# Performance work log

Hardware: AMD Instinct MI355X
Metric: run time of the kernel (lower is better)

Reference implementation:

```python
import jax, jax.numpy as jnp
import numpy as np

NUM_EXPS = [8, 16, 64, 256, 1024]
KS = [4, 4, 32, 32, 256]
HIDDEN = 256
OUT_DIM = 3
IN_DIM = 2
N_IMGS = 2
N_COORDS = 1024


def setup_inputs() -> dict:
    key = jax.random.key(0)
    ks = jax.random.split(key, 16)
    inp = {}
    inp["raw_gates"] = jax.random.normal(ks[0], (N_IMGS, sum(NUM_EXPS)), jnp.float32)
    inp["coords"] = jax.random.uniform(ks[1], (N_COORDS, IN_DIM), jnp.float32, -1.0, 1.0)
    fan_in = [IN_DIM] + [HIDDEN] * 4
    fan_out = [HIDDEN * e for e in NUM_EXPS[:-1]] + [OUT_DIM * NUM_EXPS[-1]]
    for i, (fi, fo) in enumerate(zip(fan_in, fan_out)):
        # first_layer_sine_init / sine_init weight scales from the torch module
        bound = (1.0 / fi) if i == 0 else (np.sqrt(6.0 / fi) / 30.0)
        inp[f"W{i}"] = jax.random.uniform(ks[2 + 2 * i], (fo, fi), jnp.float32, -bound, bound)
        bb = 1.0 / np.sqrt(fi)  # torch nn.Linear default bias init
        inp[f"b{i}"] = jax.random.uniform(ks[3 + 2 * i], (fo,), jnp.float32, -bb, bb)
    return inp


def _topk_gate(g, k):
    # torch: topk(|g|, k+1) -> keep top k, gather signed values, scatter into zeros
    _, idx = jax.lax.top_k(jnp.abs(g), min(k + 1, g.shape[1]))
    idx = idx[:, :k]
    vals = jnp.take_along_axis(g, idx, axis=1)
    rows = jnp.arange(g.shape[0])[:, None]
    return jnp.zeros_like(g).at[rows, idx].set(vals)


def _forward(raw_gates, coords, Ws, bs):
    offs = np.cumsum([0] + NUM_EXPS)
    gates = [_topk_gate(raw_gates[:, offs[i]:offs[i + 1]], KS[i]) for i in range(len(NUM_EXPS))]
    Ni = raw_gates.shape[0]
    Nc = coords.shape[0]
    E0 = NUM_EXPS[0]
    # layer 0: shared experts, combine = sparse gates @ expert outputs (== MoECombiner scatter-add)
    h = jnp.sin(30.0 * (coords @ Ws[0].T + bs[0]))            # [Nc, H*E0]
    h = h.reshape(Nc, HIDDEN, E0).transpose(2, 0, 1).reshape(E0, Nc * HIDDEN)  # [E0, Nc*H]
    x = (gates[0] @ h).reshape(Ni, Nc, HIDDEN)                # [Ni, Nc, H]
    for i in range(1, len(NUM_EXPS)):
        E = NUM_EXPS[i]
        h = x @ Ws[i].T + bs[i]                               # [Ni, Nc, d*E]
        if i < len(NUM_EXPS) - 1:
            h = jnp.sin(30.0 * h)
            d = HIDDEN
        else:
            d = OUT_DIM                                       # last layer: no activation
        h = h.reshape(Ni, Nc, d, E)
        x = jnp.einsum('icde,ie->icd', h, gates[i])           # bmm(gate, experts)
    return x


def reference(raw_gates, coords, W0, b0, W1, b1, W2, b2, W3, b3, W4, b4):
    return _forward(raw_gates, coords, (W0, W1, W2, W3, W4), (b0, b1, b2, b3, b4))
```

## Files before the change

kernel.cpp:

```cpp
#include <hip/hip_runtime.h>
#include <math.h>

#define NC 1024
#define HID 256
#define NI 2

typedef _Float16 f16x8 __attribute__((ext_vector_type(8)));
typedef float f32x4 __attribute__((ext_vector_type(4)));
using gvoid = __attribute__((address_space(1))) const void;
using lvoid = __attribute__((address_space(3))) void;

#define LO_SCALE 2048.0f
#define LO_INV (1.0f / 2048.0f)

__global__ __launch_bounds__(1024) void gate_kernel(const float* __restrict__ rg,
                                                    int* __restrict__ gidx,
                                                    float* __restrict__ gval)
{
    const int EDAT[5] = {8, 16, 64, 256, 1024};
    const int KDAT[5] = {4, 4, 32, 32, 256};
    const int OFF[5]  = {0, 8, 24, 88, 344};
    const int level = blockIdx.x, img = blockIdx.y;
    const int E = EDAT[level], K = KDAT[level], off = OFF[level];
    __shared__ float ga[1024];
    const float* src = rg + img * 1368 + off;
    const int t = threadIdx.x;
    if (t < E) ga[t] = src[t];
    __syncthreads();
    if (t < E) {
        const float v = ga[t];
        const float a = fabsf(v);
        int rank = 0;
#pragma unroll 8
        for (int j = 0; j < E; j++) {
            float aj = fabsf(ga[j]);
            rank += (aj > a) || (aj == a && j < t);
        }
        if (rank < K) {
            int base = (level * 2 + img) * 256;
            gidx[base + rank] = t;
            gval[base + rank] = v;
        }
    }
}

__global__ __launch_bounds__(256) void layer0_kernel(const float* __restrict__ coords,
                                                     const float* __restrict__ W0,
                                                     const float* __restrict__ b0,
                                                     const int* __restrict__ gidx,
                                                     const float* __restrict__ gval,
                                                     float* __restrict__ xout)
{
    const int c = blockIdx.x, img = blockIdx.y, h = threadIdx.x;
    __shared__ int gi[4];
    __shared__ float gv[4];
    if (h < 4) {
        int base = (0 * 2 + img) * 256;
        gi[h] = gidx[base + h];
        gv[h] = gval[base + h];
    }
    __syncthreads();
    const float c0 = coords[c * 2], c1 = coords[c * 2 + 1];
    float s = 0.f;
#pragma unroll
    for (int k = 0; k < 4; k++) {
        int row = h * 8 + gi[k];
        s += gv[k] * __sinf(30.f * (c0 * W0[row * 2] + c1 * W0[row * 2 + 1] + b0[row]));
    }
    xout[((size_t)img * NC + c) * HID + h] = s;
}

__global__ __launch_bounds__(256) void xpack_kernel(const float* __restrict__ x,
                                                    _Float16* __restrict__ Ap)
{
    const int mt = blockIdx.x, img = blockIdx.y, sa = blockIdx.z;
    const int t = threadIdx.x;
    const int c = t & 63, r0 = t >> 6;
    const float* xb = x + ((size_t)img * NC + mt * 64) * HID;
    _Float16* aph = Ap + ((size_t)(img * 16 + mt) * 8 + sa) * 4096;
    _Float16* apl = aph + 4 * 4096;
    const int kk = sa * 64 + c;
#pragma unroll
    for (int rr = 0; rr < 64; rr += 4) {
        int r = rr + r0;
        float v = xb[r * HID + kk];
        _Float16 h = (_Float16)v;
        int idx = r * 64 + (c ^ ((r & 7) << 3));
        aph[idx] = h;
        apl[idx] = (_Float16)((v - (float)h) * LO_SCALE);
    }
}

__global__ __launch_bounds__(256) void wpack_kernel(const float* __restrict__ W,
                                                    const float* __restrict__ bias,
                                                    const int* __restrict__ gidx,
                                                    const float* __restrict__ gval,
                                                    int level, int E, int lgK,
                                                    _Float16* __restrict__ Bp,
                                                    float* __restrict__ biasP,
                                                    float* __restrict__ gvP,
                                                    int ntiles)
{
    const int ntile = blockIdx.x, img = blockIdx.y, sa = blockIdx.z;
    const int t = threadIdx.x;
    const int N = ntiles * 64;
    __shared__ int wrowS[64];
    const int base = (level * 2 + img) * 256;
    if (t < 64) {
        int n = ntile * 64 + t;
        int dd = n >> lgK, k = n & ((1 << lgK) - 1);
        int wrow = dd * E + gidx[base + k];
        wrowS[t] = wrow;
        if (sa == 0) {
            biasP[img * N + n] = bias[wrow];
            gvP[img * N + n] = gval[base + k];
        }
    }
    __syncthreads();
    const int c = t & 63, r0 = t >> 6;
    const int kk = sa * 64 + c;
    _Float16* bph = Bp + ((size_t)(img * ntiles + ntile) * 8 + sa) * 4096;
    _Float16* bpl = bph + 4 * 4096;
#pragma unroll
    for (int rr = 0; rr < 64; rr += 4) {
        int r = rr + r0;
        float v = W[(size_t)wrowS[r] * HID + kk];
        _Float16 h = (_Float16)v;
        int idx = r * 64 + (c ^ ((r & 7) << 3));
        bph[idx] = h;
        bpl[idx] = (_Float16)((v - (float)h) * LO_SCALE);
    }
}

template <int KGRP, int NTB>
__global__ __launch_bounds__(256, 1) void mid_mfma_kernel(const _Float16* __restrict__ Ap,
                                                          const _Float16* __restrict__ Bp,
                                                          const float* __restrict__ biasP,
                                                          const float* __restrict__ gvP,
                                                          float* __restrict__ x_out)
{
    constexpr int NTBX = NTB / 8;
    const int b = blockIdx.x;
    const int q = b & 7;
    const int j = b >> 3;
    const int mtp = j & 7;
    const int img = (j >> 3) & 1;
    const int ntl = j >> 4;
    const int nt = q * NTBX + ntl;

    const int tid = threadIdx.x;
    const int wave = tid >> 6, lane = tid & 63;
    const int wm = wave & 1, wn = wave >> 1;
    const int l15 = lane & 15, lhi = lane >> 4;

    __shared__ __align__(16) char lds[131072];
    float* S = (float*)lds;

    const int ntiles = NTB * 2;
    const int N = NTB * 128;
    const _Float16* ag = Ap + ((size_t)(img * 16 + mtp * 2) * 8) * 4096;
    const _Float16* bg = Bp + ((size_t)(img * ntiles + nt * 2) * 8) * 4096;

    const _Float16* sbase = (wave & 2) ? bg : ag;
    const int planeAdd = (wave & 1) ? 4 : 0;
    auto stage = [&](int bufoff, int p) {
#pragma unroll
        for (int qq = 0; qq < 16; ++qq) {
            const _Float16* g = sbase + (size_t)(qq >> 3) * 32768
                              + (planeAdd + p) * 4096 + (qq & 7) * 512 + lane * 8;
            __builtin_amdgcn_global_load_lds((gvoid*)g,
                (lvoid*)(lds + bufoff + wave * 16384 + qq * 1024), 16, 0, 0);
        }
    };

    f32x4 acc[4][4], accL[4][4];
#pragma unroll
    for (int mi = 0; mi < 4; mi++)
#pragma unroll
        for (int ni = 0; ni < 4; ni++) { acc[mi][ni] = (f32x4)0.f; accL[mi][ni] = (f32x4)0.f; }

    stage(0, 0);

#pragma unroll
    for (int p = 0; p < 4; ++p) {
        const int cur = (p & 1) * 65536;
        asm volatile("s_waitcnt vmcnt(0)" ::: "memory");
        __syncthreads();
        if (p < 3) stage(65536 - cur, p + 1);

#pragma unroll
        for (int ks = 0; ks < 2; ++ks) {
            f16x8 ah[4], al[4], bh[4], bl[4];
#pragma unroll
            for (int mi = 0; mi < 4; ++mi) {
                int row = wm * 64 + mi * 16 + l15;
                int off = (row >> 6) * 8192 + (row & 63) * 128
                        + (((lhi + 4 * ks) ^ (row & 7)) * 16);
                ah[mi] = *(const f16x8*)(lds + cur + off);
                al[mi] = *(const f16x8*)(lds + cur + 16384 + off);
            }
#pragma unroll
            for (int ni = 0; ni < 4; ++ni) {
                int row = wn * 64 + ni * 16 + l15;
                int off = (row >> 6) * 8192 + (row & 63) * 128
                        + (((lhi + 4 * ks) ^ (row & 7)) * 16);
                bh[ni] = *(const f16x8*)(lds + cur + 32768 + off);
                bl[ni] = *(const f16x8*)(lds + cur + 49152 + off);
            }
#pragma unroll
            for (int mi = 0; mi < 4; ++mi)
#pragma unroll
                for (int ni = 0; ni < 4; ++ni)
                    acc[mi][ni] = __builtin_amdgcn_mfma_f32_16x16x32_f16(ah[mi], bh[ni],
                                                                         acc[mi][ni], 0, 0, 0);
#pragma unroll
            for (int mi = 0; mi < 4; ++mi)
#pragma unroll
                for (int ni = 0; ni < 4; ++ni)
                    accL[mi][ni] = __builtin_amdgcn_mfma_f32_16x16x32_f16(al[mi], bh[ni],
                                                                          accL[mi][ni], 0, 0, 0);
#pragma unroll
            for (int mi = 0; mi < 4; ++mi)
#pragma unroll
                for (int ni = 0; ni < 4; ++ni)
                    accL[mi][ni] = __builtin_amdgcn_mfma_f32_16x16x32_f16(ah[mi], bl[ni],
                                                                          accL[mi][ni], 0, 0, 0);
        }
    }
    __syncthreads();

#pragma unroll
    for (int mi = 0; mi < 4; ++mi)
#pragma unroll
        for (int ni = 0; ni < 4; ++ni) {
            int n = wn * 64 + ni * 16 + l15;
            int gn = nt * 128 + n;
            float bv = biasP[img * N + gn];
            float gv = gvP[img * N + gn];
#pragma unroll
            for (int r = 0; r < 4; ++r) {
                int m = wm * 64 + mi * 16 + lhi * 4 + r;
                float val = acc[mi][ni][r] + accL[mi][ni][r] * LO_INV;
                S[m * 129 + n] = gv * __sinf(30.f * (val + bv));
            }
        }
    __syncthreads();

    float* xo = x_out + ((size_t)img * NC + mtp * 128) * HID;
    if (KGRP == 32) {
#pragma unroll
        for (int rep = 0; rep < 2; ++rep) {
            int idx = rep * 256 + tid;
            int m = idx >> 2, d = idx & 3;
            float s = 0.f;
#pragma unroll
            for (int jj = 0; jj < 32; ++jj) s += S[m * 129 + d * 32 + ((jj + d * 8) & 31)];
            xo[m * HID + nt * 4 + d] = s;
        }
    } else {
#pragma unroll
        for (int rep = 0; rep < 16; ++rep) {
            int idx = rep * 256 + tid;
            int m = idx >> 5, dl = idx & 31;
            const float* Sp = S + m * 129 + dl * 4;
            xo[m * HID + nt * 32 + dl] = Sp[0] + Sp[1] + Sp[2] + Sp[3];
        }
    }
}

__global__ __launch_bounds__(256) void l4combine_kernel(const float* __restrict__ W4,
                                                        const float* __restrict__ b4,
                                                        const int* __restrict__ gidx,
                                                        const float* __restrict__ gval,
                                                        float* __restrict__ Weff,
                                                        float* __restrict__ beff)
{
    const int d = blockIdx.x, img = blockIdx.y;
    const int t = threadIdx.x;
    const int base = (4 * 2 + img) * 256;
    __shared__ int rows[256];
    __shared__ float gs[256];
    __shared__ float bred[256];
    int e = gidx[base + t];
    float g = gval[base + t];
    rows[t] = (d * 1024 + e) * 256;
    gs[t] = g;
    bred[t] = g * b4[d * 1024 + e];
    __syncthreads();
    float acc = 0.f;
#pragma unroll 4
    for (int k = 0; k < 256; ++k)
        acc = fmaf(gs[k], W4[(size_t)rows[k] + t], acc);
    Weff[(img * 3 + d) * 256 + t] = acc;
    for (int s = 128; s > 0; s >>= 1) {
        if (t < s) bred[t] += bred[t + s];
        __syncthreads();
    }
    if (t == 0) beff[img * 3 + d] = bred[0];
}

__global__ __launch_bounds__(256) void l4apply_kernel(const float* __restrict__ x_in,
                                                      const float* __restrict__ Weff,
                                                      const float* __restrict__ beff,
                                                      float* __restrict__ out)
{
    const int img = blockIdx.y;
    const int c = blockIdx.x * 256 + threadIdx.x;
    __shared__ float ws[3][256];
    __shared__ float bs[3];
    const int t = threadIdx.x;
    if (t < 192) {
        int d = t / 64, k4 = t % 64;
        *(float4*)&ws[d][k4 * 4] = *(const float4*)(Weff + (img * 3 + d) * 256 + k4 * 4);
    }
    if (t < 3) bs[t] = beff[img * 3 + t];
    __syncthreads();
    const float* xb = x_in + ((size_t)img * NC + c) * HID;
    float a0 = 0.f, a1 = 0.f, a2 = 0.f;
#pragma unroll 4
    for (int k = 0; k < 256; k += 4) {
        const float4 xv = *(const float4*)(xb + k);
        const float4 w0 = *(const float4*)&ws[0][k];
        const float4 w1 = *(const float4*)&ws[1][k];
        const float4 w2 = *(const float4*)&ws[2][k];
        a0 += xv.x * w0.x + xv.y * w0.y + xv.z * w0.z + xv.w * w0.w;
        a1 += xv.x * w1.x + xv.y * w1.y + xv.z * w1.z + xv.w * w1.w;
        a2 += xv.x * w2.x + xv.y * w2.y + xv.z * w2.z + xv.w * w2.w;
    }
    float* o = out + ((size_t)img * NC + c) * 3;
    o[0] = a0 + bs[0];
    o[1] = a1 + bs[1];
    o[2] = a2 + bs[2];
}

extern "C" void kernel_launch(void* const* d_in, const int* in_sizes, int n_in,
                              void* d_out, int out_size, void* d_ws, size_t ws_size,
                              hipStream_t stream)
{
    const float* rg     = (const float*)d_in[0];
    const float* coords = (const float*)d_in[1];
    const float* W0 = (const float*)d_in[2];
    const float* b0 = (const float*)d_in[3];
    const float* W1 = (const float*)d_in[4];
    const float* b1 = (const float*)d_in[5];
    const float* W2 = (const float*)d_in[6];
    const float* b2 = (const float*)d_in[7];
    const float* W3 = (const float*)d_in[8];
    const float* b3 = (const float*)d_in[9];
    const float* W4 = (const float*)d_in[10];
    const float* b4 = (const float*)d_in[11];
    float* out = (float*)d_out;

    char* ws = (char*)d_ws;
    int*      gidx  = (int*)ws;
    float*    gval  = (float*)(ws + 10240);
    float*    xA    = (float*)(ws + 20480);
    float*    xB    = (float*)(ws + 2117632);
    _Float16* Ap    = (_Float16*)(ws + 4214784);
    _Float16* Bp    = (_Float16*)(ws + 6311936);
    float*    biasP = (float*)(ws + 23089152);
    float*    gvP   = (float*)(ws + 23154688);
    float*    Weff  = (float*)(ws + 23220224);
    float*    beff  = (float*)(ws + 23228416);

    gate_kernel<<<dim3(5, 2), 1024, 0, stream>>>(rg, gidx, gval);
    l4combine_kernel<<<dim3(3, 2), 256, 0, stream>>>(W4, b4, gidx, gval, Weff, beff);
    layer0_kernel<<<dim3(NC, NI), 256, 0, stream>>>(coords, W0, b0, gidx, gval, xA);

    xpack_kernel<<<dim3(16, 2, 4), 256, 0, stream>>>(xA, Ap);
    wpack_kernel<<<dim3(16, 2, 4), 256, 0, stream>>>(W1, b1, gidx, gval, 1, 16, 2, Bp, biasP, gvP, 16);
    mid_mfma_kernel<4, 8><<<128, 256, 0, stream>>>(Ap, Bp, biasP, gvP, xB);

    xpack_kernel<<<dim3(16, 2, 4), 256, 0, stream>>>(xB, Ap);
    wpack_kernel<<<dim3(128, 2, 4), 256, 0, stream>>>(W2, b2, gidx, gval, 2, 64, 5, Bp, biasP, gvP, 128);
    mid_mfma_kernel<32, 64><<<1024, 256, 0, stream>>>(Ap, Bp, biasP, gvP, xA);

    xpack_kernel<<<dim3(16, 2, 4), 256, 0, stream>>>(xA, Ap);
    wpack_kernel<<<dim3(128, 2, 4), 256, 0, stream>>>(W3, b3, gidx, gval, 3, 256, 5, Bp, biasP, gvP, 128);
    mid_mfma_kernel<32, 64><<<1024, 256, 0, stream>>>(Ap, Bp, biasP, gvP, xB);

    l4apply_kernel<<<dim3(4, 2), 256, 0, stream>>>(xB, Weff, beff, out);
}
```

Before: 312.7 us.

## Fuse activation packing into epilogues, batch weight packing, and single-buffer MFMA LDS

Layer0 and the MFMA epilogues now write the hi/lo fp16 swizzled A-operand directly, which removes the separate xpack kernels and their fp32 round trips. Weight packing for W1/W2 and the layer-4 weight combine are merged into one prep kernel, with the combine split across chunks and accumulated through atomics into buffers that the gate kernel zeroes. The MFMA kernel drops from 128KB of double-buffered LDS to a 64KB single buffer and stages the next panel after the second k-step's fragments are read. The epilogue reduction moves from an LDS scratch pass to warp shuffles. These changes cut kernel launches and memory traffic, but the single buffer gives less load/compute overlap, and the float atomics make the summation order nondeterministic.

```diff
diff --git a/kernel.cpp b/kernel.cpp
--- a/kernel.cpp
+++ b/kernel.cpp
@@ -13,9 +13,38 @@
 #define LO_SCALE 2048.0f
 #define LO_INV (1.0f / 2048.0f)
 
+#define OFF_GIDX  0
+#define OFF_GVAL  10240
+#define OFF_B1    20480
+#define OFF_G1    28672
+#define OFF_B2    36864
+#define OFF_G2    102400
+#define OFF_B3    167936
+#define OFF_G3    233472
+#define OFF_WEFF  299008
+#define OFF_BEFF  305152
+#define OFF_APA   307200
+#define OFF_APB   (OFF_APA + 2097152)
+#define OFF_BP1   (OFF_APB + 2097152)
+#define OFF_BP23  (OFF_BP1 + 2097152)
+
+__device__ __forceinline__ void pack_store(_Float16* __restrict__ ApN, int img,
+                                           int m, int h, float v)
+{
+    _Float16 hi = (_Float16)v;
+    _Float16 lo = (_Float16)((v - (float)hi) * LO_SCALE);
+    int mt = m >> 6, r = m & 63;
+    size_t base = ((size_t)(img * 16 + mt) * 8 + (h >> 6)) * 4096
+                + r * 64 + ((h & 63) ^ ((r & 7) << 3));
+    ApN[base] = hi;
+    ApN[base + 16384] = lo;
+}
+
 __global__ __launch_bounds__(1024) void gate_kernel(const float* __restrict__ rg,
                                                     int* __restrict__ gidx,
-                                                    float* __restrict__ gval)
+                                                    float* __restrict__ gval,
+                                                    float* __restrict__ Weff,
+                                                    float* __restrict__ beff)
 {
     const int EDAT[5] = {8, 16, 64, 256, 1024};
     const int KDAT[5] = {4, 4, 32, 32, 256};
@@ -25,6 +54,10 @@
     __shared__ float ga[1024];
     const float* src = rg + img * 1368 + off;
     const int t = threadIdx.x;
+    if (level == 0) {
+        if (t < 768) Weff[img * 768 + t] = 0.f;
+        if (t < 3) beff[img * 3 + t] = 0.f;
+    }
     if (t < E) ga[t] = src[t];
     __syncthreads();
     if (t < E) {
@@ -49,7 +82,7 @@
                                                      const float* __restrict__ b0,
                                                      const int* __restrict__ gidx,
                                                      const float* __restrict__ gval,
-                                                     float* __restrict__ xout)
+                                                     _Float16* __restrict__ ApN)
 {
     const int c = blockIdx.x, img = blockIdx.y, h = threadIdx.x;
     __shared__ int gi[4];
@@ -67,41 +100,19 @@
         int row = h * 8 + gi[k];
         s += gv[k] * __sinf(30.f * (c0 * W0[row * 2] + c1 * W0[row * 2 + 1] + b0[row]));
     }
-    xout[((size_t)img * NC + c) * HID + h] = s;
-}
-
-__global__ __launch_bounds__(256) void xpack_kernel(const float* __restrict__ x,
-                                                    _Float16* __restrict__ Ap)
-{
-    const int mt = blockIdx.x, img = blockIdx.y, sa = blockIdx.z;
-    const int t = threadIdx.x;
-    const int c = t & 63, r0 = t >> 6;
-    const float* xb = x + ((size_t)img * NC + mt * 64) * HID;
-    _Float16* aph = Ap + ((size_t)(img * 16 + mt) * 8 + sa) * 4096;
-    _Float16* apl = aph + 4 * 4096;
-    const int kk = sa * 64 + c;
-#pragma unroll
-    for (int rr = 0; rr < 64; rr += 4) {
-        int r = rr + r0;
-        float v = xb[r * HID + kk];
-        _Float16 h = (_Float16)v;
-        int idx = r * 64 + (c ^ ((r & 7) << 3));
-        aph[idx] = h;
-        apl[idx] = (_Float16)((v - (float)h) * LO_SCALE);
-    }
-}
-
-__global__ __launch_bounds__(256) void wpack_kernel(const float* __restrict__ W,
-                                                    const float* __restrict__ bias,
-                                                    const int* __restrict__ gidx,
-                                                    const float* __restrict__ gval,
-                                                    int level, int E, int lgK,
-                                                    _Float16* __restrict__ Bp,
-                                                    float* __restrict__ biasP,
-                                                    float* __restrict__ gvP,
-                                                    int ntiles)
-{
-    const int ntile = blockIdx.x, img = blockIdx.y, sa = blockIdx.z;
+    pack_store(ApN, img, c, h, s);
+}
+
+__device__ __forceinline__ void wpack_body(const float* __restrict__ W,
+                                           const float* __restrict__ bias,
+                                           const int* __restrict__ gidx,
+                                           const float* __restrict__ gval,
+                                           int level, int E, int lgK, int ntiles,
+                                           _Float16* __restrict__ Bp,
+                                           float* __restrict__ biasP,
+                                           float* __restrict__ gvP,
+                                           int ntile, int img, int sa)
+{
     const int t = threadIdx.x;
     const int N = ntiles * 64;
     __shared__ int wrowS[64];
@@ -132,12 +143,76 @@
     }
 }
 
-template <int KGRP, int NTB>
+__global__ __launch_bounds__(256) void prep_kernel(const float* __restrict__ W1,
+                                                   const float* __restrict__ b1,
+                                                   const float* __restrict__ W2,
+                                                   const float* __restrict__ b2,
+                                                   const float* __restrict__ W4,
+                                                   const float* __restrict__ b4,
+                                                   const int* __restrict__ gidx,
+                                                   const float* __restrict__ gval,
+                                                   _Float16* __restrict__ Bp1,
+                                                   float* __restrict__ bias1,
+                                                   float* __restrict__ gv1,
+                                                   _Float16* __restrict__ Bp23,
+                                                   float* __restrict__ bias2,
+                                                   float* __restrict__ gv2,
+                                                   float* __restrict__ Weff,
+                                                   float* __restrict__ beff)
+{
+    const int b = blockIdx.x;
+    if (b < 128) {
+        int ntile = b & 15, img = (b >> 4) & 1, sa = b >> 5;
+        wpack_body(W1, b1, gidx, gval, 1, 16, 2, 16, Bp1, bias1, gv1, ntile, img, sa);
+    } else if (b < 1152) {
+        int s = b - 128;
+        int ntile = s & 127, img = (s >> 7) & 1, sa = s >> 8;
+        wpack_body(W2, b2, gidx, gval, 2, 64, 5, 128, Bp23, bias2, gv2, ntile, img, sa);
+    } else {
+        const int idx = b - 1152;
+        const int d = idx % 3, img = (idx / 3) % 2, ck = idx / 6;
+        const int t = threadIdx.x;
+        __shared__ float gs[32];
+        __shared__ int rows[32];
+        const int base = (4 * 2 + img) * 256 + ck * 32;
+        if (t < 32) {
+            gs[t] = gval[base + t];
+            rows[t] = (d * 1024 + gidx[base + t]) * 256;
+        }
+        __syncthreads();
+        float acc = 0.f;
+#pragma unroll 8
+        for (int k = 0; k < 32; ++k)
+            acc = fmaf(gs[k], W4[(size_t)rows[k] + t], acc);
+        atomicAdd(&Weff[(img * 3 + d) * 256 + t], acc);
+        if (t == 0) {
+            float bb = 0.f;
+            for (int k = 0; k < 32; ++k)
+                bb += gs[k] * b4[d * 1024 + gidx[base + k]];
+            atomicAdd(&beff[img * 3 + d], bb);
+        }
+    }
+}
+
+__global__ __launch_bounds__(256) void wpack3_kernel(const float* __restrict__ W,
+                                                     const float* __restrict__ bias,
+                                                     const int* __restrict__ gidx,
+                                                     const float* __restrict__ gval,
+                                                     _Float16* __restrict__ Bp,
+                                                     float* __restrict__ biasP,
+                                                     float* __restrict__ gvP)
+{
+    wpack_body(W, bias, gidx, gval, 3, 256, 5, 128, Bp, biasP, gvP,
+               blockIdx.x, blockIdx.y, blockIdx.z);
+}
+
+template <int KGRP, int NTB, bool PACK>
 __global__ __launch_bounds__(256, 1) void mid_mfma_kernel(const _Float16* __restrict__ Ap,
                                                           const _Float16* __restrict__ Bp,
-                                                          const float* __restrict__ biasP,
-                                                          const float* __restrict__ gvP,
-                                                          float* __restrict__ x_out)
+                                                          const float* __restrict__ biasPp,
+                                                          const float* __restrict__ gvPp,
+                                                          float* __restrict__ xout,
+                                                          _Float16* __restrict__ ApN)
 {
     constexpr int NTBX = NTB / 8;
     const int b = blockIdx.x;
@@ -153,8 +228,7 @@
     const int wm = wave & 1, wn = wave >> 1;
     const int l15 = lane & 15, lhi = lane >> 4;
 
-    __shared__ __align__(16) char lds[131072];
-    float* S = (float*)lds;
+    __shared__ __align__(16) char lds[65536];
 
     const int ntiles = NTB * 2;
     const int N = NTB * 128;
@@ -163,13 +237,13 @@
 
     const _Float16* sbase = (wave & 2) ? bg : ag;
     const int planeAdd = (wave & 1) ? 4 : 0;
-    auto stage = [&](int bufoff, int p) {
+    auto stage = [&](int p) {
 #pragma unroll
         for (int qq = 0; qq < 16; ++qq) {
             const _Float16* g = sbase + (size_t)(qq >> 3) * 32768
                               + (planeAdd + p) * 4096 + (qq & 7) * 512 + lane * 8;
             __builtin_amdgcn_global_load_lds((gvoid*)g,
-                (lvoid*)(lds + bufoff + wave * 16384 + qq * 1024), 16, 0, 0);
+                (lvoid*)(lds + wave * 16384 + qq * 1024), 16, 0, 0);
         }
     };
 
@@ -179,124 +253,163 @@
 #pragma unroll
         for (int ni = 0; ni < 4; ni++) { acc[mi][ni] = (f32x4)0.f; accL[mi][ni] = (f32x4)0.f; }
 
-    stage(0, 0);
+    stage(0);
 
 #pragma unroll
     for (int p = 0; p < 4; ++p) {
-        const int cur = (p & 1) * 65536;
         asm volatile("s_waitcnt vmcnt(0)" ::: "memory");
         __syncthreads();
-        if (p < 3) stage(65536 - cur, p + 1);
-
-#pragma unroll
-        for (int ks = 0; ks < 2; ++ks) {
-            f16x8 ah[4], al[4], bh[4], bl[4];
-#pragma unroll
-            for (int mi = 0; mi < 4; ++mi) {
-                int row = wm * 64 + mi * 16 + l15;
-                int off = (row >> 6) * 8192 + (row & 63) * 128
-                        + (((lhi + 4 * ks) ^ (row & 7)) * 16);
-                ah[mi] = *(const f16x8*)(lds + cur + off);
-                al[mi] = *(const f16x8*)(lds + cur + 16384 + off);
-            }
-#pragma unroll
-            for (int ni = 0; ni < 4; ++ni) {
-                int row = wn * 64 + ni * 16 + l15;
-                int off = (row >> 6) * 8192 + (row & 63) * 128
-                        + (((lhi + 4 * ks) ^ (row & 7)) * 16);
-                bh[ni] = *(const f16x8*)(lds + cur + 32768 + off);
-                bl[ni] = *(const f16x8*)(lds + cur + 49152 + off);
-            }
+        f16x8 ah[2][4], al[2][4], bh[2][4], bl[2][4];
+#pragma unroll
+        for (int mi = 0; mi < 4; ++mi) {
+            int row = wm * 64 + mi * 16 + l15;
+            int off = (row >> 6) * 8192 + (row & 63) * 128 + ((lhi ^ (row & 7)) * 16);
+            ah[0][mi] = *(const f16x8*)(lds + off);
+            al[0][mi] = *(const f16x8*)(lds + 16384 + off);
+        }
+#pragma unroll
+        for (int ni = 0; ni < 4; ++ni) {
+            int row = wn * 64 + ni * 16 + l15;
+            int off = (row >> 6) * 8192 + (row & 63) * 128 + ((lhi ^ (row & 7)) * 16);
+            bh[0][ni] = *(const f16x8*)(lds + 32768 + off);
+            bl[0][ni] = *(const f16x8*)(lds + 49152 + off);
+        }
+#pragma unroll
+        for (int mi = 0; mi < 4; ++mi)
+#pragma unroll
+            for (int ni = 0; ni < 4; ++ni)
+                acc[mi][ni] = __builtin_amdgcn_mfma_f32_16x16x32_f16(ah[0][mi], bh[0][ni],
+                                                                     acc[mi][ni], 0, 0, 0);
+#pragma unroll
+        for (int mi = 0; mi < 4; ++mi)
+#pragma unroll
+            for (int ni = 0; ni < 4; ++ni)
+                accL[mi][ni] = __builtin_amdgcn_mfma_f32_16x16x32_f16(al[0][mi], bh[0][ni],
+                                                                      accL[mi][ni], 0, 0, 0);
+#pragma unroll
+        for (int mi = 0; mi < 4; ++mi)
+#pragma unroll
+            for (int ni = 0; ni < 4; ++ni)
+                accL[mi][ni] = __builtin_amdgcn_mfma_f32_16x16x32_f16(ah[0][mi], bl[0][ni],
+                                                                      accL[mi][ni], 0, 0, 0);
+#pragma unroll
+        for (int mi = 0; mi < 4; ++mi) {
+            int row = wm * 64 + mi * 16 + l15;
+            int off = (row >> 6) * 8192 + (row & 63) * 128 + ((((lhi + 4)) ^ (row & 7)) * 16);
+            ah[1][mi] = *(const f16x8*)(lds + off);
+            al[1][mi] = *(const f16x8*)(lds + 16384 + off);
+        }
+#pragma unroll
+        for (int ni = 0; ni < 4; ++ni) {
+            int row = wn * 64 + ni * 16 + l15;
+            int off = (row >> 6) * 8192 + (row & 63) * 128 + ((((lhi + 4)) ^ (row & 7)) * 16);
+            bh[1][ni] = *(const f16x8*)(lds + 32768 + off);
+            bl[1][ni] = *(const f16x8*)(lds + 49152 + off);
+        }
+        __syncthreads();
+        if (p < 3) stage(p + 1);
+#pragma unroll
+        for (int mi = 0; mi < 4; ++mi)
+#pragma unroll
+            for (int ni = 0; ni < 4; ++ni)
+                acc[mi][ni] = __builtin_amdgcn_mfma_f32_16x16x32_f16(ah[1][mi], bh[1][ni],
+                                                                     acc[mi][ni], 0, 0, 0);
+#pragma unroll
+        for (int mi = 0; mi < 4; ++mi)
+#pragma unroll
+            for (int ni = 0; ni < 4; ++ni)
+                accL[mi][ni] = __builtin_amdgcn_mfma_f32_16x16x32_f16(al[1][mi], bh[1][ni],
+                                                                      accL[mi][ni], 0, 0, 0);
+#pragma unroll
+        for (int mi = 0; mi < 4; ++mi)
+#pragma unroll
+            for (int ni = 0; ni < 4; ++ni)
+                accL[mi][ni] = __builtin_amdgcn_mfma_f32_16x16x32_f16(ah[1][mi], bl[1][ni],
+                                                                      accL[mi][ni], 0, 0, 0);
+    }
+
+    const int mbase = mtp * 128 + wm * 64;
+    if (KGRP == 32) {
+        float red[4][2][4];
+#pragma unroll
+        for (int mi = 0; mi < 4; ++mi)
+#pragma unroll
+            for (int pp = 0; pp < 2; ++pp)
+#pragma unroll
+                for (int r = 0; r < 4; ++r) red[mi][pp][r] = 0.f;
+#pragma unroll
+        for (int ni = 0; ni < 4; ++ni) {
+            int gn = nt * 128 + wn * 64 + ni * 16 + l15;
+            float bv = biasPp[img * N + gn];
+            float gvv = gvPp[img * N + gn];
+#pragma unroll
+            for (int mi = 0; mi < 4; ++mi)
+#pragma unroll
+                for (int r = 0; r < 4; ++r) {
+                    float val = acc[mi][ni][r] + accL[mi][ni][r] * LO_INV;
+                    red[mi][ni >> 1][r] += gvv * __sinf(30.f * (val + bv));
+                }
+        }
+#pragma unroll
+        for (int mask = 1; mask <= 8; mask <<= 1)
+#pragma unroll
+            for (int mi = 0; mi < 4; ++mi)
+#pragma unroll
+                for (int pp = 0; pp < 2; ++pp)
+#pragma unroll
+                    for (int r = 0; r < 4; ++r)
+                        red[mi][pp][r] += __shfl_xor(red[mi][pp][r], mask);
+        if (l15 == 0) {
+#pragma unroll
+            for (int mi = 0; mi < 4; ++mi)
+#pragma unroll
+                for (int pp = 0; pp < 2; ++pp)
+#pragma unroll
+                    for (int r = 0; r < 4; ++r) {
+                        int m = mbase + mi * 16 + lhi * 4 + r;
+                        int h = nt * 4 + wn * 2 + pp;
+                        if (PACK) pack_store(ApN, img, m, h, red[mi][pp][r]);
+                        else xout[((size_t)img * NC + m) * HID + h] = red[mi][pp][r];
+                    }
+        }
+    } else {
+        float e[4][4][4];
+#pragma unroll
+        for (int ni = 0; ni < 4; ++ni) {
+            int gn = nt * 128 + wn * 64 + ni * 16 + l15;
+            float bv = biasPp[img * N + gn];
+            float gvv = gvPp[img * N + gn];
+#pragma unroll
+            for (int mi = 0; mi < 4; ++mi)
+#pragma unroll
+                for (int r = 0; r < 4; ++r) {
+                    float val = acc[mi][ni][r] + accL[mi][ni][r] * LO_INV;
+                    e[mi][ni][r] = gvv * __sinf(30.f * (val + bv));
+                }
+        }
+#pragma unroll
+        for (int mask = 1; mask <= 2; mask <<= 1)
 #pragma unroll
             for (int mi = 0; mi < 4; ++mi)
 #pragma unroll
                 for (int ni = 0; ni < 4; ++ni)
-                    acc[mi][ni] = __builtin_amdgcn_mfma_f32_16x16x32_f16(ah[mi], bh[ni],
-                                                                         acc[mi][ni], 0, 0, 0);
+#pragma unroll
+                    for (int r = 0; r < 4; ++r)
+                        e[mi][ni][r] += __shfl_xor(e[mi][ni][r], mask);
+        if ((l15 & 3) == 0) {
 #pragma unroll
             for (int mi = 0; mi < 4; ++mi)
 #pragma unroll
                 for (int ni = 0; ni < 4; ++ni)
-                    accL[mi][ni] = __builtin_amdgcn_mfma_f32_16x16x32_f16(al[mi], bh[ni],
-                                                                          accL[mi][ni], 0, 0, 0);
-#pragma unroll
-            for (int mi = 0; mi < 4; ++mi)
-#pragma unroll
-                for (int ni = 0; ni < 4; ++ni)
-                    accL[mi][ni] = __builtin_amdgcn_mfma_f32_16x16x32_f16(ah[mi], bl[ni],
-                                                                          accL[mi][ni], 0, 0, 0);
-        }
-    }
-    __syncthreads();
-
-#pragma unroll
-    for (int mi = 0; mi < 4; ++mi)
-#pragma unroll
-        for (int ni = 0; ni < 4; ++ni) {
-            int n = wn * 64 + ni * 16 + l15;
-            int gn = nt * 128 + n;
-            float bv = biasP[img * N + gn];
-            float gv = gvP[img * N + gn];
-#pragma unroll
-            for (int r = 0; r < 4; ++r) {
-                int m = wm * 64 + mi * 16 + lhi * 4 + r;
-                float val = acc[mi][ni][r] + accL[mi][ni][r] * LO_INV;
-                S[m * 129 + n] = gv * __sinf(30.f * (val + bv));
-            }
-        }
-    __syncthreads();
-
-    float* xo = x_out + ((size_t)img * NC + mtp * 128) * HID;
-    if (KGRP == 32) {
-#pragma unroll
-        for (int rep = 0; rep < 2; ++rep) {
-            int idx = rep * 256 + tid;
-            int m = idx >> 2, d = idx & 3;
-            float s = 0.f;
-#pragma unroll
-            for (int jj = 0; jj < 32; ++jj) s += S[m * 129 + d * 32 + ((jj + d * 8) & 31)];
-            xo[m * HID + nt * 4 + d] = s;
-        }
-    } else {
-#pragma unroll
-        for (int rep = 0; rep < 16; ++rep) {
-            int idx = rep * 256 + tid;
-            int m = idx >> 5, dl = idx & 31;
-            const float* Sp = S + m * 129 + dl * 4;
-            xo[m * HID + nt * 32 + dl] = Sp[0] + Sp[1] + Sp[2] + Sp[3];
-        }
-    }
-}
-
-__global__ __launch_bounds__(256) void l4combine_kernel(const float* __restrict__ W4,
-                                                        const float* __restrict__ b4,
-                                                        const int* __restrict__ gidx,
-                                                        const float* __restrict__ gval,
-                                                        float* __restrict__ Weff,
-                                                        float* __restrict__ beff)
-{
-    const int d = blockIdx.x, img = blockIdx.y;
-    const int t = threadIdx.x;
-    const int base = (4 * 2 + img) * 256;
-    __shared__ int rows[256];
-    __shared__ float gs[256];
-    __shared__ float bred[256];
-    int e = gidx[base + t];
-    float g = gval[base + t];
-    rows[t] = (d * 1024 + e) * 256;
-    gs[t] = g;
-    bred[t] = g * b4[d * 1024 + e];
-    __syncthreads();
-    float acc = 0.f;
-#pragma unroll 4
-    for (int k = 0; k < 256; ++k)
-        acc = fmaf(gs[k], W4[(size_t)rows[k] + t], acc);
-    Weff[(img * 3 + d) * 256 + t] = acc;
-    for (int s = 128; s > 0; s >>= 1) {
-        if (t < s) bred[t] += bred[t + s];
-        __syncthreads();
-    }
-    if (t == 0) beff[img * 3 + d] = bred[0];
+#pragma unroll
+                    for (int r = 0; r < 4; ++r) {
+                        int m = mbase + mi * 16 + lhi * 4 + r;
+                        int h = nt * 32 + wn * 16 + ni * 4 + (l15 >> 2);
+                        if (PACK) pack_store(ApN, img, m, h, e[mi][ni][r]);
+                        else xout[((size_t)img * NC + m) * HID + h] = e[mi][ni][r];
+                    }
+        }
+    }
 }
 
 __global__ __launch_bounds__(256) void l4apply_kernel(const float* __restrict__ x_in,
@@ -352,32 +465,31 @@
     float* out = (float*)d_out;
 
     char* ws = (char*)d_ws;
-    int*      gidx  = (int*)ws;
-    float*    gval  = (float*)(ws + 10240);
-    float*    xA    = (float*)(ws + 20480);
-    float*    xB    = (float*)(ws + 2117632);
-    _Float16* Ap    = (_Float16*)(ws + 4214784);
-    _Float16* Bp    = (_Float16*)(ws + 6311936);
-    float*    biasP = (float*)(ws + 23089152);
-    float*    gvP   = (float*)(ws + 23154688);
-    float*    Weff  = (float*)(ws + 23220224);
-    float*    beff  = (float*)(ws + 23228416);
-
-    gate_kernel<<<dim3(5, 2), 1024, 0, stream>>>(rg, gidx, gval);
-    l4combine_kernel<<<dim3(3, 2), 256, 0, stream>>>(W4, b4, gidx, gval, Weff, beff);
-    layer0_kernel<<<dim3(NC, NI), 256, 0, stream>>>(coords, W0, b0, gidx, gval, xA);
-
-    xpack_kernel<<<dim3(16, 2, 4), 256, 0, stream>>>(xA, Ap);
-    wpack_kernel<<<dim3(16, 2, 4), 256, 0, stream>>>(W1, b1, gidx, gval, 1, 16, 2, Bp, biasP, gvP, 16);
-    mid_mfma_kernel<4, 8><<<128, 256, 0, stream>>>(Ap, Bp, biasP, gvP, xB);
-
-    xpack_kernel<<<dim3(16, 2, 4), 256, 0, stream>>>(xB, Ap);
-    wpack_kernel<<<dim3(128, 2, 4), 256, 0, stream>>>(W2, b2, gidx, gval, 2, 64, 5, Bp, biasP, gvP, 128);
-    mid_mfma_kernel<32, 64><<<1024, 256, 0, stream>>>(Ap, Bp, biasP, gvP, xA);
-
-    xpack_kernel<<<dim3(16, 2, 4), 256, 0, stream>>>(xA, Ap);
-    wpack_kernel<<<dim3(128, 2, 4), 256, 0, stream>>>(W3, b3, gidx, gval, 3, 256, 5, Bp, biasP, gvP, 128);
-    mid_mfma_kernel<32, 64><<<1024, 256, 0, stream>>>(Ap, Bp, biasP, gvP, xB);
+    int*      gidx  = (int*)(ws + OFF_GIDX);
+    float*    gval  = (float*)(ws + OFF_GVAL);
+    float*    bias1 = (float*)(ws + OFF_B1);
+    float*    gv1   = (float*)(ws + OFF_G1);
+    float*    bias2 = (float*)(ws + OFF_B2);
+    float*    gv2   = (float*)(ws + OFF_G2);
+    float*    bias3 = (float*)(ws + OFF_B3);
+    float*    gv3   = (float*)(ws + OFF_G3);
+    float*    Weff  = (float*)(ws + OFF_WEFF);
+    float*    beff  = (float*)(ws + OFF_BEFF);
+    _Float16* ApA   = (_Float16*)(ws + OFF_APA);
+    _Float16* ApB   = (_Float16*)(ws + OFF_APB);
+    _Float16* Bp1   = (_Float16*)(ws + OFF_BP1);
+    float*    xB    = (float*)(ws + OFF_BP1);
+    _Float16* Bp23  = (_Float16*)(ws + OFF_BP23);
+
+    gate_kernel<<<dim3(5, 2), 1024, 0, stream>>>(rg, gidx, gval, Weff, beff);
+    prep_kernel<<<1200, 256, 0, stream>>>(W1, b1, W2, b2, W4, b4, gidx, gval,
+                                          Bp1, bias1, gv1, Bp23, bias2, gv2, Weff, beff);
+    layer0_kernel<<<dim3(NC, NI), 256, 0, stream>>>(coords, W0, b0, gidx, gval, ApA);
+
+    mid_mfma_kernel<4, 8, true><<<128, 256, 0, stream>>>(ApA, Bp1, bias1, gv1, nullptr, ApB);
+    mid_mfma_kernel<32, 64, true><<<1024, 256, 0, stream>>>(ApB, Bp23, bias2, gv2, nullptr, ApA);
+    wpack3_kernel<<<dim3(128, 2, 4), 256, 0, stream>>>(W3, b3, gidx, gval, Bp23, bias3, gv3);
+    mid_mfma_kernel<32, 64, false><<<1024, 256, 0, stream>>>(ApA, Bp23, bias3, gv3, xB, nullptr);
 
     l4apply_kernel<<<dim3(4, 2), 256, 0, stream>>>(xB, Weff, beff, out);
 }
```

New measurement: 312.4 us. No clear change (-0.1%).
